# Kernel tuning notes

Measured on AMD Instinct MI355X. Metric: run time of the kernel, lower is better.

Reference implementation:

```python
import jax, jax.numpy as jnp
import numpy as np

N = 100000        # nodes
E = 3200000       # edges (avg degree 32)
D = 16            # feature dim
LAM = 1.0
ALP = 1.0 / (LAM + 1.0)   # alp=0 default -> 1/(lam+1)
PROP_STEP = 5


def setup_inputs() -> dict:
    key = jax.random.key(0)
    k1, k2, k3 = jax.random.split(key, 3)
    edge_index = jax.random.randint(k1, (2, E), 0, N, dtype=jnp.int32)
    X = jax.random.normal(k2, (N, D), dtype=jnp.float32)
    train_mask = jax.random.randint(k3, (N,), 0, 2, dtype=jnp.int32) > 0
    return {"edge_index": edge_index, "X": X, "train_mask": train_mask}


def reference(edge_index, X, train_mask):
    src, dst = edge_index[0], edge_index[1]
    # g.edata['w'] = ones; g.ndata['deg'] = in_degrees
    deg = jax.ops.segment_sum(jnp.ones((E,), X.dtype), dst, num_segments=N)
    dinv = jnp.where(deg > 0, jax.lax.rsqrt(jnp.maximum(deg, 1.0)), 0.0)  # D^{-1/2}, 0-deg -> 0

    def norm_AX(Y):
        # D^{-1/2} A D^{-1/2} Y  via gather over src, scatter-add into dst
        h = (Y * dinv[:, None])[src]                       # [E, D]
        agg = jax.ops.segment_sum(h, dst, num_segments=N)  # [N, D]
        return agg * dinv[:, None]

    mask = train_mask[:, None]
    Y = X
    for _ in range(PROP_STEP):
        # PropagateNoPrecond: (1 - alp - alp*lam) Y + alp*lam * Ahat Y + alp * X
        Y = (1.0 - ALP - ALP * LAM) * Y + (ALP * LAM) * norm_AX(Y) + ALP * X
        # error=True branch: post_step clamp then reset train nodes to X
        Y = jnp.clip(Y, -1.0, 1.0)
        Y = jnp.where(mask, X, Y)
    return Y
```

## Files before the change

### kernel.cpp

```cpp
#include <hip/hip_runtime.h>

#define NN 100000
#define NE 3200000
#define DD 16
#define NB 782
#define NBP 1024
#define CHUNK 8192
#define NCHUNK ((NE + CHUNK - 1) / CHUNK)
#define PREPB ((NN + NBP - 1) / NBP)
#define BCAP2 4864
#define BMW 3128

constexpr float LAM   = 1.0f;
constexpr float ALP   = 1.0f / (LAM + 1.0f);
constexpr float GAMMA = ALP * LAM;
constexpr float S0    = 127.0f / 6.0f;
constexpr float INVS0 = 6.0f / 127.0f;
constexpr float INVS1 = 1.0f / 127.0f;

__global__ __launch_bounds__(NBP) void bucket_scatter(
        const int* __restrict__ srcs, const int* __restrict__ dsts,
        int* __restrict__ bcnt, unsigned int* __restrict__ pk,
        const int* __restrict__ mask, unsigned long long* __restrict__ bm64,
        int* __restrict__ ulist, int* __restrict__ ucount) {
    int t = threadIdx.x;

    if (blockIdx.x >= NCHUNK) {
        int n = (int)(blockIdx.x - NCHUNK) * NBP + t;
        int lane = t & 63;
        bool m = (n < NN) && (mask[n] != 0);
        unsigned long long balm = __ballot(m);
        int w = n >> 6;
        if (lane == 0 && w < 1564) bm64[w] = balm;
        bool u = (n < NN) && !m;
        unsigned long long bal = __ballot(u);
        int cnt = __popcll(bal);
        int base = 0;
        if (lane == 0 && cnt > 0) base = atomicAdd(ucount, cnt);
        base = __shfl(base, 0, 64);
        if (u) ulist[base + __popcll(bal & ((1ull << lane) - 1ull))] = n;
        return;
    }

    __shared__ int lh[NBP];
    __shared__ int off[NBP];
    __shared__ int gb[NBP];
    __shared__ int wred[16];
    __shared__ unsigned long long spair[CHUNK];
    int base = blockIdx.x * CHUNK;
    int n = NE - base; if (n > CHUNK) n = CHUNK;

    lh[t] = 0;
    __syncthreads();

    int e0 = 8 * t;
    int dreg[8];
    bool full = (e0 + 8 <= n);
    if (full) {
        int4 a = *(const int4*)&dsts[base + e0];
        int4 bq = *(const int4*)&dsts[base + e0 + 4];
        dreg[0] = a.x;  dreg[1] = a.y;  dreg[2] = a.z;  dreg[3] = a.w;
        dreg[4] = bq.x; dreg[5] = bq.y; dreg[6] = bq.z; dreg[7] = bq.w;
        #pragma unroll
        for (int k = 0; k < 8; ++k) atomicAdd(&lh[dreg[k] >> 7], 1);
    } else {
        #pragma unroll
        for (int k = 0; k < 8; ++k) {
            int i = e0 + k;
            dreg[k] = (i < n) ? dsts[base + i] : -1;
        }
        #pragma unroll
        for (int k = 0; k < 8; ++k)
            if (dreg[k] >= 0) atomicAdd(&lh[dreg[k] >> 7], 1);
    }
    __syncthreads();

    int v = lh[t];
    int x = v;
    #pragma unroll
    for (int s = 1; s < 64; s <<= 1) {
        int y = __shfl_up(x, s, 64);
        if ((t & 63) >= s) x += y;
    }
    if ((t & 63) == 63) wred[t >> 6] = x;
    __syncthreads();
    if (t < 16) {
        int ww = wred[t];
        int xx = ww;
        #pragma unroll
        for (int s = 1; s < 16; s <<= 1) {
            int y = __shfl_up(xx, s, 16);
            if (t >= s) xx += y;
        }
        wred[t] = xx - ww;
    }
    __syncthreads();
    x += wred[t >> 6];
    int cnt  = v;
    int excl = x - v;
    off[t] = excl;
    if (cnt > 0) gb[t] = t * BCAP2 + atomicAdd(&bcnt[t], cnt) - excl;
    __syncthreads();

    if (full) {
        int4 a = *(const int4*)&srcs[base + e0];
        int4 bq = *(const int4*)&srcs[base + e0 + 4];
        int sreg[8];
        sreg[0] = a.x;  sreg[1] = a.y;  sreg[2] = a.z;  sreg[3] = a.w;
        sreg[4] = bq.x; sreg[5] = bq.y; sreg[6] = bq.z; sreg[7] = bq.w;
        #pragma unroll
        for (int k = 0; k < 8; ++k) {
            unsigned int d = (unsigned int)dreg[k];
            int p = atomicAdd(&off[d >> 7], 1);
            spair[p] = ((unsigned long long)d << 32) | (unsigned int)sreg[k];
        }
    } else {
        #pragma unroll
        for (int k = 0; k < 8; ++k) {
            int i = e0 + k;
            if (i < n) {
                unsigned int d = (unsigned int)dreg[k];
                unsigned int s = (unsigned int)srcs[base + i];
                int p = atomicAdd(&off[d >> 7], 1);
                spair[p] = ((unsigned long long)d << 32) | s;
            }
        }
    }
    __syncthreads();

    unsigned long long wv[8];
    #pragma unroll
    for (int k = 0; k < 8; ++k) {
        int p = t + k * NBP;
        wv[k] = (p < n) ? spair[p] : 0ull;
    }
    #pragma unroll
    for (int k = 0; k < 8; ++k) {
        int p = t + k * NBP;
        if (p < n) {
            unsigned int d = (unsigned int)(wv[k] >> 32);
            int bb = (int)(d >> 7);
            pk[gb[bb] + p] = ((d & 127u) << 17) | (unsigned int)wv[k];
        }
    }
}

static __device__ inline unsigned int qb8(float xv, float sc) {
    float q = fminf(fmaxf(xv * sc, -127.0f), 127.0f);
    return (unsigned int)(__float2int_rn(q) + 128) & 255u;
}

__global__ void fine_csr(unsigned int* __restrict__ pk,
                         const int* __restrict__ bcnt,
                         const float* __restrict__ X,
                         const unsigned int* __restrict__ bitmap,
                         int* __restrict__ row_start, int* __restrict__ midp,
                         int* __restrict__ dendp,
                         float* __restrict__ dinv,
                         unsigned char* __restrict__ Za,
                         unsigned char* __restrict__ Zb,
                         float* __restrict__ Y) {
    __shared__ int lh[256], off[256];
    __shared__ int wred[4];
    __shared__ float sdi[128];
    __shared__ unsigned int bmp[BMW];
    __shared__ int sbuf[BCAP2];
    int b  = blockIdx.x;
    int t  = threadIdx.x;
    int b0 = b * BCAP2;
    int cnt = bcnt[b];
    lh[t] = 0;
    for (int i0 = 4 * t; i0 < BMW; i0 += 1024) {
        uint4 q = *(const uint4*)&bitmap[i0];
        *(uint4*)&bmp[i0] = q;
    }
    __syncthreads();

    for (int i0 = 4 * t; i0 < cnt; i0 += 1024) {
        if (i0 + 4 <= cnt) {
            uint4 q = *(const uint4*)&pk[b0 + i0];
            unsigned int vv[4] = {q.x, q.y, q.z, q.w};
            #pragma unroll
            for (int k = 0; k < 4; ++k) {
                unsigned int s = vv[k] & 0x1FFFFu;
                int mb = (bmp[s >> 5] >> (s & 31)) & 1;
                atomicAdd(&lh[((vv[k] >> 17) << 1) | (mb ? 0 : 1)], 1);
            }
        } else {
            for (int k = 0; k < 4; ++k) {
                int i = i0 + k;
                if (i < cnt) {
                    unsigned int v = pk[b0 + i];
                    unsigned int s = v & 0x1FFFFu;
                    int mb = (bmp[s >> 5] >> (s & 31)) & 1;
                    atomicAdd(&lh[((v >> 17) << 1) | (mb ? 0 : 1)], 1);
                }
            }
        }
    }
    __syncthreads();
    int v = lh[t];
    int x = v;
    #pragma unroll
    for (int s = 1; s < 64; s <<= 1) {
        int y = __shfl_up(x, s, 64);
        if ((t & 63) >= s) x += y;
    }
    if ((t & 63) == 63) wred[t >> 6] = x;
    __syncthreads();
    if (t < 4) {
        int ww = wred[t];
        int xx = ww;
        #pragma unroll
        for (int s = 1; s < 4; s <<= 1) {
            int y = __shfl_up(xx, s, 4);
            if (t >= s) xx += y;
        }
        wred[t] = xx - ww;
    }
    __syncthreads();
    x += wred[t >> 6];
    off[t] = x;
    int myexcl = x - v;
    __syncthreads();
    if (t < 128) {
        int cs = lh[2 * t], cd = lh[2 * t + 1];
        int es = off[2 * t] - cs;
        int ed = off[2 * t + 1] - cd;
        int c  = cs + cd;
        int dst = (b << 7) + t;
        float di = (c > 0) ? rsqrtf((float)c) : 0.0f;
        sdi[t] = di;
        if (dst < NN) {
            row_start[dst] = b0 + es;
            midp[dst]      = b0 + ed;
            dendp[dst]     = b0 + ed + cd;
            dinv[dst]      = di;
        }
    }
    __syncthreads();
    off[t] = myexcl;
    __syncthreads();

    for (int i0 = 4 * t; i0 < cnt; i0 += 1024) {
        if (i0 + 4 <= cnt) {
            uint4 q = *(const uint4*)&pk[b0 + i0];
            unsigned int vv[4] = {q.x, q.y, q.z, q.w};
            #pragma unroll
            for (int k = 0; k < 4; ++k) {
                unsigned int s = vv[k] & 0x1FFFFu;
                int mb = (bmp[s >> 5] >> (s & 31)) & 1;
                int p = atomicAdd(&off[((vv[k] >> 17) << 1) | (mb ? 0 : 1)], 1);
                sbuf[p] = (int)s;
            }
        } else {
            for (int k = 0; k < 4; ++k) {
                int i = i0 + k;
                if (i < cnt) {
                    unsigned int v2 = pk[b0 + i];
                    unsigned int s = v2 & 0x1FFFFu;
                    int mb = (bmp[s >> 5] >> (s & 31)) & 1;
                    int p = atomicAdd(&off[((v2 >> 17) << 1) | (mb ? 0 : 1)], 1);
                    sbuf[p] = (int)s;
                }
            }
        }
    }
    __syncthreads();

    for (int i0 = 4 * t; i0 < cnt; i0 += 1024) {
        if (i0 + 4 <= cnt) {
            int4 q = *(const int4*)&sbuf[i0];
            *(int4*)&pk[b0 + i0] = q;
        } else {
            for (int k = 0; k < 4; ++k) {
                int i = i0 + k;
                if (i < cnt) pk[b0 + i] = (unsigned int)sbuf[i];
            }
        }
    }

    {
        int ldst = t >> 1;
        int ff0  = (t & 1) * 8;
        int dst  = (b << 7) + ldst;
        if (dst < NN) {
            float4 xa = *(const float4*)&X[dst * DD + ff0];
            float4 xb = *(const float4*)&X[dst * DD + ff0 + 4];
            float sc = sdi[ldst] * S0;
            unsigned int w0 = qb8(xa.x, sc) | (qb8(xa.y, sc) << 8) |
                              (qb8(xa.z, sc) << 16) | (qb8(xa.w, sc) << 24);
            unsigned int w1 = qb8(xb.x, sc) | (qb8(xb.y, sc) << 8) |
                              (qb8(xb.z, sc) << 16) | (qb8(xb.w, sc) << 24);
            *(uint2*)(Za + dst * DD + ff0) = make_uint2(w0, w1);
            if ((bmp[dst >> 5] >> (dst & 31)) & 1) {
                *(float4*)&Y[dst * DD + ff0]     = xa;
                *(float4*)&Y[dst * DD + ff0 + 4] = xb;
            }
        }
    }
    if (b == 0 && t < DD) {
        Za[NN * DD + t] = 128;
        Zb[NN * DD + t] = 128;
    }
}

static __device__ inline void fold16(float* acc, int ln) {
    {
        int sel = ln & 1;
        #pragma unroll
        for (int k = 0; k < 8; ++k) {
            float mine   = sel ? acc[k + 8] : acc[k];
            float theirs = sel ? acc[k]     : acc[k + 8];
            acc[k] = mine + __shfl_xor(theirs, 1, 16);
        }
    }
    {
        int sel = (ln >> 1) & 1;
        #pragma unroll
        for (int k = 0; k < 4; ++k) {
            float mine   = sel ? acc[k + 4] : acc[k];
            float theirs = sel ? acc[k]     : acc[k + 4];
            acc[k] = mine + __shfl_xor(theirs, 2, 16);
        }
    }
    {
        int sel = (ln >> 2) & 1;
        #pragma unroll
        for (int k = 0; k < 2; ++k) {
            float mine   = sel ? acc[k + 2] : acc[k];
            float theirs = sel ? acc[k]     : acc[k + 2];
            acc[k] = mine + __shfl_xor(theirs, 4, 16);
        }
    }
    {
        int sel = (ln >> 3) & 1;
        float mine   = sel ? acc[1] : acc[0];
        float theirs = sel ? acc[0] : acc[1];
        acc[0] = mine + __shfl_xor(theirs, 8, 16);
    }
}

static __device__ inline void accum16(const unsigned int* __restrict__ csr,
                                      const uint4* __restrict__ Zt,
                                      int lo, int hi, int ln, float* acc) {
    int p = lo + ln;
    int s = (p < hi) ? (int)__builtin_nontemporal_load((const int*)&csr[p]) : NN;
    for (int i = lo; i < hi; i += 16) {
        uint4 r = Zt[s];
        int pn = i + 16 + ln;
        int sn = (pn < hi) ? (int)__builtin_nontemporal_load((const int*)&csr[pn]) : NN;
        acc[0]  += (float)(r.x & 255u);         acc[1]  += (float)((r.x >> 8) & 255u);
        acc[2]  += (float)((r.x >> 16) & 255u); acc[3]  += (float)(r.x >> 24);
        acc[4]  += (float)(r.y & 255u);         acc[5]  += (float)((r.y >> 8) & 255u);
        acc[6]  += (float)((r.y >> 16) & 255u); acc[7]  += (float)(r.y >> 24);
        acc[8]  += (float)(r.z & 255u);         acc[9]  += (float)((r.z >> 8) & 255u);
        acc[10] += (float)((r.z >> 16) & 255u); acc[11] += (float)(r.z >> 24);
        acc[12] += (float)(r.w & 255u);         acc[13] += (float)((r.w >> 8) & 255u);
        acc[14] += (float)((r.w >> 16) & 255u); acc[15] += (float)(r.w >> 24);
        s = sn;
    }
}

__global__ void gather_kernel(const unsigned int* __restrict__ csr,
                              const int* __restrict__ row_start,
                              const int* __restrict__ midp,
                              const int* __restrict__ dendp,
                              const float* __restrict__ dinv,
                              const float* __restrict__ X,
                              float* __restrict__ Sst,
                              const int* __restrict__ ulist,
                              const int* __restrict__ ucount,
                              const unsigned char* __restrict__ Zrow,
                              unsigned char* __restrict__ Zout,
                              float* __restrict__ Yo,
                              float invS, int first, int last) {
    int tid = blockIdx.x * blockDim.x + threadIdx.x;
    int idx = tid >> 4;
    int ln  = tid & 15;
    if (idx >= *ucount) return;
    int node = ulist[idx];
    int mid = midp[node], hi = dendp[node];
    float di = dinv[node];
    int fp = 8 * (ln & 1) + 4 * ((ln >> 1) & 1) + 2 * ((ln >> 2) & 1) + ((ln >> 3) & 1);
    const uint4* Zt = (const uint4*)Zrow;

    float s0;
    float g = GAMMA * di * invS;
    if (first) {
        int lo = row_start[node];
        float accS[16];
        #pragma unroll
        for (int k = 0; k < 16; ++k) accS[k] = 0.0f;
        accum16(csr, Zt, lo, mid, ln, accS);
        fold16(accS, ln);
        int nchS = (mid - lo + 15) >> 4;
        float bias = 2048.0f * (float)nchS;
        float x0 = __builtin_nontemporal_load(&X[node * DD + fp]);
        s0 = g * (accS[0] - bias) + ALP * x0;
        Sst[node * DD + fp] = s0;
    } else {
        s0 = Sst[node * DD + fp];
    }

    float acc[16];
    #pragma unroll
    for (int k = 0; k < 16; ++k) acc[k] = 0.0f;
    accum16(csr, Zt, mid, hi, ln, acc);
    fold16(acc, ln);
    int nchD = (hi - mid + 15) >> 4;
    float v0 = s0 + g * (acc[0] - 2048.0f * (float)nchD);
    v0 = fminf(fmaxf(v0, -1.0f), 1.0f);
    if (last) {
        Yo[node * DD + fp] = v0;
    } else {
        int q0 = __float2int_rn(v0 * di * 127.0f) + 128;
        Zout[node * DD + fp] = (unsigned char)q0;
    }
}

extern "C" void kernel_launch(void* const* d_in, const int* in_sizes, int n_in,
                              void* d_out, int out_size, void* d_ws, size_t ws_size,
                              hipStream_t stream) {
    const int*   edge_index = (const int*)d_in[0];
    const float* X          = (const float*)d_in[1];
    const int*   mask       = (const int*)d_in[2];

    const int* srcs = edge_index;
    const int* dsts = edge_index + NE;

    float* Y = (float*)d_out;

    unsigned char* Za = (unsigned char*)d_ws;
    unsigned char* Zb = Za + (NN + 1) * DD;
    float* Sst        = (float*)(Zb + (NN + 1) * DD);
    unsigned int* pk  = (unsigned int*)(Sst + NN * DD);
    int*   bcnt      = (int*)(pk + NB * BCAP2);
    int*   ucount    = bcnt + NBP;
    int*   pad       = ucount + 1;
    unsigned int* bitmap = (unsigned int*)(pad + 3);
    int*   ulist     = (int*)(bitmap + BMW);
    int*   midp      = ulist + NN;
    int*   dendp     = midp + NN;
    int*   row_start = dendp + NN;
    float* dinv      = (float*)(row_start + NN);

    (void)hipMemsetAsync(bcnt, 0, (NBP + 4) * sizeof(int), stream);

    bucket_scatter<<<NCHUNK + PREPB, NBP, 0, stream>>>(
        srcs, dsts, bcnt, pk, mask, (unsigned long long*)bitmap, ulist, ucount);
    fine_csr<<<NB, 256, 0, stream>>>(pk, bcnt, X, bitmap, row_start, midp, dendp,
                                     dinv, Za, Zb, Y);

    const unsigned char* zin  = Za;
    unsigned char*       zout = Zb;
    for (int t = 0; t < 5; ++t) {
        int first = (t == 0);
        int last  = (t == 4);
        gather_kernel<<<(NN * 16) / 256, 256, 0, stream>>>(
            pk, row_start, midp, dendp, dinv, X, Sst, ulist, ucount,
            zin, zout, Y, first ? INVS0 : INVS1, first, last);
        const unsigned char* tmp = zout;
        zout = (unsigned char*)zin;
        zin  = tmp;
    }
}
```

Before: 121.7 us.

## Pack per-node gather descriptors and reuse atomic ranks in bucketing

Replaces the separate ulist/midp/dendp/dinv arrays with one uint4 descriptor per unmasked node, indexed densely, so each gather thread does a single 16-byte load instead of several dependent loads. The histogram atomics now return ranks that are reused in the scatter pass, which removes the second round of LDS atomics in both bucket_scatter and fine_csr. Global bucket counters are padded to separate cache lines, and the unmasked-node list is built with one global atomic per block. It also drops the nontemporal loads on CSR indices. The trade-off is extra LDS for the rank buffer and a slightly more complex prep path.

Result: faster. 107.5 us (-11.7%).

```diff
diff --git a/kernel.cpp b/kernel.cpp
--- a/kernel.cpp
+++ b/kernel.cpp
@@ -22,31 +22,41 @@
         const int* __restrict__ srcs, const int* __restrict__ dsts,
         int* __restrict__ bcnt, unsigned int* __restrict__ pk,
         const int* __restrict__ mask, unsigned long long* __restrict__ bm64,
-        int* __restrict__ ulist, int* __restrict__ ucount) {
-    int t = threadIdx.x;
-
-    if (blockIdx.x >= NCHUNK) {
-        int n = (int)(blockIdx.x - NCHUNK) * NBP + t;
-        int lane = t & 63;
-        bool m = (n < NN) && (mask[n] != 0);
-        unsigned long long balm = __ballot(m);
-        int w = n >> 6;
-        if (lane == 0 && w < 1564) bm64[w] = balm;
-        bool u = (n < NN) && !m;
-        unsigned long long bal = __ballot(u);
-        int cnt = __popcll(bal);
-        int base = 0;
-        if (lane == 0 && cnt > 0) base = atomicAdd(ucount, cnt);
-        base = __shfl(base, 0, 64);
-        if (u) ulist[base + __popcll(bal & ((1ull << lane) - 1ull))] = n;
-        return;
-    }
-
+        int* __restrict__ uidx, int* __restrict__ ucount) {
     __shared__ int lh[NBP];
     __shared__ int off[NBP];
     __shared__ int gb[NBP];
     __shared__ int wred[16];
     __shared__ unsigned long long spair[CHUNK];
+    int t = threadIdx.x;
+
+    if (blockIdx.x >= NCHUNK) {
+        int n0 = (int)(blockIdx.x - NCHUNK) * NBP + t;
+        int lane = t & 63;
+        bool m = (n0 < NN) && (mask[n0] != 0);
+        unsigned long long balm = __ballot(m);
+        int w = n0 >> 6;
+        if (lane == 0 && w < 1564) bm64[w] = balm;
+        bool u = (n0 < NN) && !m;
+        unsigned long long bal = __ballot(u);
+        int cnt = __popcll(bal);
+        if (lane == 0) wred[t >> 6] = cnt;
+        __syncthreads();
+        if (t == 0) {
+            int s = 0;
+            #pragma unroll
+            for (int w2 = 0; w2 < 16; ++w2) { int c = wred[w2]; wred[w2] = s; s += c; }
+            gb[0] = (s > 0) ? atomicAdd(ucount, s) : 0;
+        }
+        __syncthreads();
+        if (u) {
+            int pos = gb[0] + wred[t >> 6] +
+                      __popcll(bal & ((1ull << lane) - 1ull));
+            uidx[n0] = pos;
+        }
+        return;
+    }
+
     int base = blockIdx.x * CHUNK;
     int n = NE - base; if (n > CHUNK) n = CHUNK;
 
@@ -55,6 +65,7 @@
 
     int e0 = 8 * t;
     int dreg[8];
+    int rk[8];
     bool full = (e0 + 8 <= n);
     if (full) {
         int4 a = *(const int4*)&dsts[base + e0];
@@ -62,7 +73,7 @@
         dreg[0] = a.x;  dreg[1] = a.y;  dreg[2] = a.z;  dreg[3] = a.w;
         dreg[4] = bq.x; dreg[5] = bq.y; dreg[6] = bq.z; dreg[7] = bq.w;
         #pragma unroll
-        for (int k = 0; k < 8; ++k) atomicAdd(&lh[dreg[k] >> 7], 1);
+        for (int k = 0; k < 8; ++k) rk[k] = atomicAdd(&lh[dreg[k] >> 7], 1);
     } else {
         #pragma unroll
         for (int k = 0; k < 8; ++k) {
@@ -71,7 +82,7 @@
         }
         #pragma unroll
         for (int k = 0; k < 8; ++k)
-            if (dreg[k] >= 0) atomicAdd(&lh[dreg[k] >> 7], 1);
+            rk[k] = (dreg[k] >= 0) ? atomicAdd(&lh[dreg[k] >> 7], 1) : 0;
     }
     __syncthreads();
 
@@ -99,7 +110,7 @@
     int cnt  = v;
     int excl = x - v;
     off[t] = excl;
-    if (cnt > 0) gb[t] = t * BCAP2 + atomicAdd(&bcnt[t], cnt) - excl;
+    if (cnt > 0) gb[t] = t * BCAP2 + atomicAdd(&bcnt[t << 4], cnt) - excl;
     __syncthreads();
 
     if (full) {
@@ -111,7 +122,7 @@
         #pragma unroll
         for (int k = 0; k < 8; ++k) {
             unsigned int d = (unsigned int)dreg[k];
-            int p = atomicAdd(&off[d >> 7], 1);
+            int p = off[d >> 7] + rk[k];
             spair[p] = ((unsigned long long)d << 32) | (unsigned int)sreg[k];
         }
     } else {
@@ -121,7 +132,7 @@
             if (i < n) {
                 unsigned int d = (unsigned int)dreg[k];
                 unsigned int s = (unsigned int)srcs[base + i];
-                int p = atomicAdd(&off[d >> 7], 1);
+                int p = off[d >> 7] + rk[k];
                 spair[p] = ((unsigned long long)d << 32) | s;
             }
         }
@@ -154,9 +165,9 @@
                          const int* __restrict__ bcnt,
                          const float* __restrict__ X,
                          const unsigned int* __restrict__ bitmap,
-                         int* __restrict__ row_start, int* __restrict__ midp,
-                         int* __restrict__ dendp,
-                         float* __restrict__ dinv,
+                         const int* __restrict__ uidx,
+                         int* __restrict__ row_start,
+                         uint4* __restrict__ ndesc,
                          unsigned char* __restrict__ Za,
                          unsigned char* __restrict__ Zb,
                          float* __restrict__ Y) {
@@ -165,10 +176,11 @@
     __shared__ float sdi[128];
     __shared__ unsigned int bmp[BMW];
     __shared__ int sbuf[BCAP2];
+    __shared__ unsigned short rnk[BCAP2];
     int b  = blockIdx.x;
     int t  = threadIdx.x;
     int b0 = b * BCAP2;
-    int cnt = bcnt[b];
+    int cnt = bcnt[b << 4];
     lh[t] = 0;
     for (int i0 = 4 * t; i0 < BMW; i0 += 1024) {
         uint4 q = *(const uint4*)&bitmap[i0];
@@ -184,7 +196,8 @@
             for (int k = 0; k < 4; ++k) {
                 unsigned int s = vv[k] & 0x1FFFFu;
                 int mb = (bmp[s >> 5] >> (s & 31)) & 1;
-                atomicAdd(&lh[((vv[k] >> 17) << 1) | (mb ? 0 : 1)], 1);
+                int key = (int)((vv[k] >> 17) << 1) | (mb ? 0 : 1);
+                rnk[i0 + k] = (unsigned short)atomicAdd(&lh[key], 1);
             }
         } else {
             for (int k = 0; k < 4; ++k) {
@@ -193,7 +206,8 @@
                     unsigned int v = pk[b0 + i];
                     unsigned int s = v & 0x1FFFFu;
                     int mb = (bmp[s >> 5] >> (s & 31)) & 1;
-                    atomicAdd(&lh[((v >> 17) << 1) | (mb ? 0 : 1)], 1);
+                    int key = (int)((v >> 17) << 1) | (mb ? 0 : 1);
+                    rnk[i] = (unsigned short)atomicAdd(&lh[key], 1);
                 }
             }
         }
@@ -233,9 +247,13 @@
         sdi[t] = di;
         if (dst < NN) {
             row_start[dst] = b0 + es;
-            midp[dst]      = b0 + ed;
-            dendp[dst]     = b0 + ed + cd;
-            dinv[dst]      = di;
+            if (!((bmp[dst >> 5] >> (dst & 31)) & 1)) {
+                int ix = uidx[dst];
+                ndesc[ix] = make_uint4((unsigned int)dst,
+                                       (unsigned int)(b0 + ed),
+                                       (unsigned int)(b0 + ed + cd),
+                                       __float_as_uint(di));
+            }
         }
     }
     __syncthreads();
@@ -250,7 +268,8 @@
             for (int k = 0; k < 4; ++k) {
                 unsigned int s = vv[k] & 0x1FFFFu;
                 int mb = (bmp[s >> 5] >> (s & 31)) & 1;
-                int p = atomicAdd(&off[((vv[k] >> 17) << 1) | (mb ? 0 : 1)], 1);
+                int key = (int)((vv[k] >> 17) << 1) | (mb ? 0 : 1);
+                int p = off[key] + (int)rnk[i0 + k];
                 sbuf[p] = (int)s;
             }
         } else {
@@ -260,7 +279,8 @@
                     unsigned int v2 = pk[b0 + i];
                     unsigned int s = v2 & 0x1FFFFu;
                     int mb = (bmp[s >> 5] >> (s & 31)) & 1;
-                    int p = atomicAdd(&off[((v2 >> 17) << 1) | (mb ? 0 : 1)], 1);
+                    int key = (int)((v2 >> 17) << 1) | (mb ? 0 : 1);
+                    int p = off[key] + (int)rnk[i];
                     sbuf[p] = (int)s;
                 }
             }
@@ -345,11 +365,11 @@
                                       const uint4* __restrict__ Zt,
                                       int lo, int hi, int ln, float* acc) {
     int p = lo + ln;
-    int s = (p < hi) ? (int)__builtin_nontemporal_load((const int*)&csr[p]) : NN;
+    int s = (p < hi) ? (int)csr[p] : NN;
     for (int i = lo; i < hi; i += 16) {
         uint4 r = Zt[s];
         int pn = i + 16 + ln;
-        int sn = (pn < hi) ? (int)__builtin_nontemporal_load((const int*)&csr[pn]) : NN;
+        int sn = (pn < hi) ? (int)csr[pn] : NN;
         acc[0]  += (float)(r.x & 255u);         acc[1]  += (float)((r.x >> 8) & 255u);
         acc[2]  += (float)((r.x >> 16) & 255u); acc[3]  += (float)(r.x >> 24);
         acc[4]  += (float)(r.y & 255u);         acc[5]  += (float)((r.y >> 8) & 255u);
@@ -364,12 +384,9 @@
 
 __global__ void gather_kernel(const unsigned int* __restrict__ csr,
                               const int* __restrict__ row_start,
-                              const int* __restrict__ midp,
-                              const int* __restrict__ dendp,
-                              const float* __restrict__ dinv,
+                              const uint4* __restrict__ ndesc,
                               const float* __restrict__ X,
                               float* __restrict__ Sst,
-                              const int* __restrict__ ulist,
                               const int* __restrict__ ucount,
                               const unsigned char* __restrict__ Zrow,
                               unsigned char* __restrict__ Zout,
@@ -379,9 +396,11 @@
     int idx = tid >> 4;
     int ln  = tid & 15;
     if (idx >= *ucount) return;
-    int node = ulist[idx];
-    int mid = midp[node], hi = dendp[node];
-    float di = dinv[node];
+    uint4 nd = ndesc[idx];
+    int node = (int)nd.x;
+    int mid  = (int)nd.y;
+    int hi   = (int)nd.z;
+    float di = __uint_as_float(nd.w);
     int fp = 8 * (ln & 1) + 4 * ((ln >> 1) & 1) + 2 * ((ln >> 2) & 1) + ((ln >> 3) & 1);
     const uint4* Zt = (const uint4*)Zrow;
 
@@ -436,21 +455,19 @@
     float* Sst        = (float*)(Zb + (NN + 1) * DD);
     unsigned int* pk  = (unsigned int*)(Sst + NN * DD);
     int*   bcnt      = (int*)(pk + NB * BCAP2);
-    int*   ucount    = bcnt + NBP;
+    int*   ucount    = bcnt + NBP * 16;
     int*   pad       = ucount + 1;
     unsigned int* bitmap = (unsigned int*)(pad + 3);
-    int*   ulist     = (int*)(bitmap + BMW);
-    int*   midp      = ulist + NN;
-    int*   dendp     = midp + NN;
-    int*   row_start = dendp + NN;
-    float* dinv      = (float*)(row_start + NN);
-
-    (void)hipMemsetAsync(bcnt, 0, (NBP + 4) * sizeof(int), stream);
+    int*   uidx      = (int*)(bitmap + BMW);
+    int*   row_start = uidx + NN;
+    uint4* ndesc     = (uint4*)(row_start + NN);
+
+    (void)hipMemsetAsync(bcnt, 0, (NBP * 16 + 4) * sizeof(int), stream);
 
     bucket_scatter<<<NCHUNK + PREPB, NBP, 0, stream>>>(
-        srcs, dsts, bcnt, pk, mask, (unsigned long long*)bitmap, ulist, ucount);
-    fine_csr<<<NB, 256, 0, stream>>>(pk, bcnt, X, bitmap, row_start, midp, dendp,
-                                     dinv, Za, Zb, Y);
+        srcs, dsts, bcnt, pk, mask, (unsigned long long*)bitmap, uidx, ucount);
+    fine_csr<<<NB, 256, 0, stream>>>(pk, bcnt, X, bitmap, uidx, row_start,
+                                     ndesc, Za, Zb, Y);
 
     const unsigned char* zin  = Za;
     unsigned char*       zout = Zb;
@@ -458,7 +475,7 @@
         int first = (t == 0);
         int last  = (t == 4);
         gather_kernel<<<(NN * 16) / 256, 256, 0, stream>>>(
-            pk, row_start, midp, dendp, dinv, X, Sst, ulist, ucount,
+            pk, row_start, ndesc, X, Sst, ucount,
             zin, zout, Y, first ? INVS0 : INVS1, first, last);
         const unsigned char* tmp = zout;
         zout = (unsigned char*)zin;
```
